# Optimization experiments

Hardware: AMD Instinct MI355X
Metric: run time of the kernel (lower is better)

Reference implementation:

```python
import jax, jax.numpy as jnp
import numpy as np

NUM_BLOCKS = 32
B, S = 8, 2048


def setup_inputs() -> dict:
    key = jax.random.key(0)
    k1, k2, k3 = jax.random.split(key, 3)
    h = jax.random.uniform(k1, (B, S, NUM_BLOCKS, 4), dtype=jnp.float32)
    W = jax.random.uniform(k2, (B, S, NUM_BLOCKS, NUM_BLOCKS), dtype=jnp.float32)
    stim = jax.random.uniform(k3, (B, S, NUM_BLOCKS), dtype=jnp.float32)
    return {"h": h, "W": W, "stim": stim}


def _step(h, W, stim):
    nb = h.shape[-2]
    eye = jnp.eye(nb, dtype=W.dtype)
    W_no_self = W * (1.0 - eye)                      # zero self-connections
    # neighbor inflow: [b,s,i,j] @ [b,s,j,c] -> [b,s,i,c]
    inflow = jnp.einsum('bsij,bsjc->bsic', W_no_self, h)
    total_w = W_no_self.sum(axis=-1, keepdims=True) + 1e-8
    neigh = inflow / total_w                          # weighted neighbor mean

    E, P, G, L = h[..., 0], h[..., 1], h[..., 2], h[..., 3]
    En, Pn, Gn, Ln = neigh[..., 0], neigh[..., 1], neigh[..., 2], neigh[..., 3]

    clamp01 = lambda x: jnp.clip(x, 0.0, 1.0)
    E_new = clamp01(E + 0.3 * stim - 0.4 * P - 0.2 * G)
    P_new = clamp01(P + 0.5 * stim + 0.3 * (Pn - P) - 0.2 * E)
    G_new = clamp01(G + 0.4 * E * (1.0 - P) + 0.2 * (Gn - G) - 0.3 * P)
    good_neighbor = 0.5 * En + 0.5 * Gn
    L_new = clamp01(L + 0.4 * good_neighbor + 0.3 * (Ln - L) - 0.3 * P)

    h_new = jnp.stack([E_new, P_new, G_new, L_new], axis=-1)  # [b,s,nb,4]

    # pairwise euclidean distance over the 4 EPGL channels (torch.cdist p=2)
    diff = h_new[..., :, None, :] - h_new[..., None, :, :]    # [b,s,nb,nb,4]
    sq = jnp.sum(diff * diff, axis=-1)
    # safe sqrt: zero distance -> 0 (matches cdist; avoids nan grads)
    h_diff = jnp.where(sq > 0, jnp.sqrt(jnp.where(sq > 0, sq, 1.0)), 0.0)

    mutual_L = 0.5 * (L_new[..., :, None] + L_new[..., None, :])
    alpha, beta = 0.1 * mutual_L, 0.05
    W_new = W + alpha * h_diff - beta * W
    W_new = jnp.clip(W_new, 0.0, 1.0) * (1.0 - eye)
    return h_new, W_new


def reference(h, W, stim):
    return _step(h, W, stim)
```

## Files before the change

kernel.cpp:

```cpp
#include <hip/hip_runtime.h>

#define NB 32
#define WAVES_PER_BLOCK 4

__device__ __forceinline__ float clamp01(float x) {
    return fminf(fmaxf(x, 0.0f), 1.0f);
}

__global__ __launch_bounds__(256, 8) void biotoken_step(
    const float* __restrict__ h,
    const float* __restrict__ W,
    const float* __restrict__ stim,
    float* __restrict__ out_h,
    float* __restrict__ out_W)
{
    const int lw    = threadIdx.x & 63;
    const int wave  = threadIdx.x >> 6;
    const int token = blockIdx.x * WAVES_PER_BLOCK + wave;
    const int i     = lw & 31;
    const int half  = lw >> 5;
    const int c0    = half * 16;

    __shared__ float s_hin [WAVES_PER_BLOCK][NB * 4];
    __shared__ float s_hnew[WAVES_PER_BLOCK][NB * 4];

    const float*  Wt  = W + (size_t)token * (NB * NB);
    const float4* wrp = (const float4*)(Wt + i * NB + c0);
    float4 wrow[4];
    wrow[0] = wrp[0];
    wrow[1] = wrp[1];
    wrow[2] = wrp[2];
    wrow[3] = wrp[3];

    if (lw < NB) {
        ((float4*)s_hin[wave])[lw] =
            ((const float4*)(h + (size_t)token * (NB * 4)))[lw];
    }
    const float sti = stim[(size_t)token * NB + i];
    __builtin_amdgcn_wave_barrier();

    const float* shin = s_hin[wave];
    const float* wf   = (const float*)wrow;

    float accE = 0.f, accP = 0.f, accG = 0.f, accL = 0.f, tot = 0.f;
    #pragma unroll
    for (int t = 0; t < 16; ++t) {
        const int j = c0 + t;
        float w = wf[t];
        w = (j == i) ? 0.0f : w;
        const float4 hj = *(const float4*)&shin[j * 4];
        accE = fmaf(w, hj.x, accE);
        accP = fmaf(w, hj.y, accP);
        accG = fmaf(w, hj.z, accG);
        accL = fmaf(w, hj.w, accL);
        tot += w;
    }
    accE += __shfl_xor(accE, 32);
    accP += __shfl_xor(accP, 32);
    accG += __shfl_xor(accG, 32);
    accL += __shfl_xor(accL, 32);
    tot  += __shfl_xor(tot,  32);

    const float inv = 1.0f / (tot + 1e-8f);
    const float En = accE * inv, Pn = accP * inv, Gn = accG * inv, Ln = accL * inv;

    const float4 hi = *(const float4*)&shin[i * 4];
    const float E = hi.x, P = hi.y, G = hi.z, L = hi.w;

    const float E_new = clamp01(E + 0.3f * sti - 0.4f * P - 0.2f * G);
    const float P_new = clamp01(P + 0.5f * sti + 0.3f * (Pn - P) - 0.2f * E);
    const float G_new = clamp01(G + 0.4f * E * (1.0f - P) + 0.2f * (Gn - G) - 0.3f * P);
    const float good  = 0.5f * En + 0.5f * Gn;
    const float L_new = clamp01(L + 0.4f * good + 0.3f * (Ln - L) - 0.3f * P);

    const float4 hr = make_float4(E_new, P_new, G_new, L_new);
    if (half == 0) {
        ((float4*)s_hnew[wave])[i] = hr;
        ((float4*)(out_h + (size_t)token * (NB * 4)))[i] = hr;
    }
    __builtin_amdgcn_wave_barrier();

    const float* shn = s_hnew[wave];
    const float  Lr  = hr.w;
    float4* outWr = (float4*)(out_W + (size_t)token * (NB * NB) + i * NB + c0);

    #pragma unroll
    for (int e = 0; e < 4; ++e) {
        float4 res;
        float* resp = &res.x;
        #pragma unroll
        for (int q = 0; q < 4; ++q) {
            const int t = 4 * e + q;
            const int j = c0 + t;
            const float4 hj = *(const float4*)&shn[j * 4];
            const float dx = hr.x - hj.x;
            const float dy = hr.y - hj.y;
            const float dz = hr.z - hj.z;
            const float dw = hr.w - hj.w;
            const float sq = dx * dx + dy * dy + dz * dz + dw * dw;
            const float dist = sqrtf(sq);
            const float mutual = 0.5f * (Lr + hj.w);
            float wn = 0.95f * wf[t] + 0.1f * mutual * dist;
            wn = clamp01(wn);
            resp[q] = (j == i) ? 0.0f : wn;
        }
        outWr[e] = res;
    }
}

extern "C" void kernel_launch(void* const* d_in, const int* in_sizes, int n_in,
                              void* d_out, int out_size, void* d_ws, size_t ws_size,
                              hipStream_t stream) {
    const float* h    = (const float*)d_in[0];
    const float* W    = (const float*)d_in[1];
    const float* stim = (const float*)d_in[2];

    const int tokens = in_sizes[2] / NB;
    float* out_h = (float*)d_out;
    float* out_W = (float*)d_out + (size_t)tokens * NB * 4;

    const int blocks = tokens / WAVES_PER_BLOCK;
    biotoken_step<<<blocks, 256, 0, stream>>>(h, W, stim, out_h, out_W);
}
```

Baseline: 142.9 us.

## Split step into h-update and W-update kernels with coalesced W access

```diff
diff --git a/kernel.cpp b/kernel.cpp
--- a/kernel.cpp
+++ b/kernel.cpp
@@ -1,36 +1,31 @@
 #include <hip/hip_runtime.h>
 
 #define NB 32
-#define WAVES_PER_BLOCK 4
+#define WPB 4
 
 __device__ __forceinline__ float clamp01(float x) {
     return fminf(fmaxf(x, 0.0f), 1.0f);
 }
 
-__global__ __launch_bounds__(256, 8) void biotoken_step(
+__global__ __launch_bounds__(256, 8) void biotoken_hnew(
     const float* __restrict__ h,
     const float* __restrict__ W,
     const float* __restrict__ stim,
-    float* __restrict__ out_h,
-    float* __restrict__ out_W)
+    float* __restrict__ out_h)
 {
     const int lw    = threadIdx.x & 63;
     const int wave  = threadIdx.x >> 6;
-    const int token = blockIdx.x * WAVES_PER_BLOCK + wave;
+    const int token = blockIdx.x * WPB + wave;
     const int i     = lw & 31;
     const int half  = lw >> 5;
     const int c0    = half * 16;
 
-    __shared__ float s_hin [WAVES_PER_BLOCK][NB * 4];
-    __shared__ float s_hnew[WAVES_PER_BLOCK][NB * 4];
+    __shared__ float s_hin[WPB][NB * 4];
 
     const float*  Wt  = W + (size_t)token * (NB * NB);
     const float4* wrp = (const float4*)(Wt + i * NB + c0);
     float4 wrow[4];
-    wrow[0] = wrp[0];
-    wrow[1] = wrp[1];
-    wrow[2] = wrp[2];
-    wrow[3] = wrp[3];
+    wrow[0] = wrp[0]; wrow[1] = wrp[1]; wrow[2] = wrp[2]; wrow[3] = wrp[3];
 
     if (lw < NB) {
         ((float4*)s_hin[wave])[lw] =
@@ -73,26 +68,58 @@
     const float good  = 0.5f * En + 0.5f * Gn;
     const float L_new = clamp01(L + 0.4f * good + 0.3f * (Ln - L) - 0.3f * P);
 
-    const float4 hr = make_float4(E_new, P_new, G_new, L_new);
     if (half == 0) {
-        ((float4*)s_hnew[wave])[i] = hr;
-        ((float4*)(out_h + (size_t)token * (NB * 4)))[i] = hr;
+        ((float4*)(out_h + (size_t)token * (NB * 4)))[i] =
+            make_float4(E_new, P_new, G_new, L_new);
+    }
+}
+
+__global__ __launch_bounds__(256, 6) void biotoken_wnew(
+    const float* __restrict__ W,
+    const float* __restrict__ hn,
+    float* __restrict__ out_W)
+{
+    const int lw    = threadIdx.x & 63;
+    const int wave  = threadIdx.x >> 6;
+    const int token = blockIdx.x * WPB + wave;
+
+    __shared__ float s_hn[WPB][NB * 4];
+
+    const float4* Wt = (const float4*)(W + (size_t)token * (NB * NB));
+    float4 wrs[4];
+    wrs[0] = Wt[0 * 64 + lw];
+    wrs[1] = Wt[1 * 64 + lw];
+    wrs[2] = Wt[2 * 64 + lw];
+    wrs[3] = Wt[3 * 64 + lw];
+
+    if (lw < NB) {
+        ((float4*)s_hn[wave])[lw] =
+            ((const float4*)(hn + (size_t)token * (NB * 4)))[lw];
     }
     __builtin_amdgcn_wave_barrier();
 
-    const float* shn = s_hnew[wave];
-    const float  Lr  = hr.w;
-    float4* outWr = (float4*)(out_W + (size_t)token * (NB * NB) + i * NB + c0);
-
+    const float* shn = s_hn[wave];
+    const int jb0 = (lw & 7) * 4;
+    float4 hjv[4];
     #pragma unroll
     for (int e = 0; e < 4; ++e) {
+        hjv[e] = *(const float4*)&shn[(jb0 + e) * 4];
+    }
+
+    float4* outWt = (float4*)(out_W + (size_t)token * (NB * NB));
+    #pragma unroll
+    for (int k = 0; k < 4; ++k) {
+        const int m = k * 64 + lw;
+        const int r = m >> 3;
+        const float4 hr = *(const float4*)&shn[r * 4];
+        const float  Lr = hr.w;
+        const float* wp = (const float*)&wrs[k];
         float4 res;
         float* resp = &res.x;
         #pragma unroll
-        for (int q = 0; q < 4; ++q) {
-            const int t = 4 * e + q;
-            const int j = c0 + t;
-            const float4 hj = *(const float4*)&shn[j * 4];
+        for (int e = 0; e < 4; ++e) {
+            const int j = jb0 + e;
+            const float4 hj = hjv[e];
             const float dx = hr.x - hj.x;
             const float dy = hr.y - hj.y;
             const float dz = hr.z - hj.z;
@@ -100,11 +127,11 @@
             const float sq = dx * dx + dy * dy + dz * dz + dw * dw;
             const float dist = sqrtf(sq);
             const float mutual = 0.5f * (Lr + hj.w);
-            float wn = 0.95f * wf[t] + 0.1f * mutual * dist;
+            float wn = 0.95f * wp[e] + 0.1f * mutual * dist;
             wn = clamp01(wn);
-            resp[q] = (j == i) ? 0.0f : wn;
+            resp[e] = (j == r) ? 0.0f : wn;
         }
-        outWr[e] = res;
+        outWt[m] = res;
     }
 }
 
@@ -119,6 +146,7 @@
     float* out_h = (float*)d_out;
     float* out_W = (float*)d_out + (size_t)tokens * NB * 4;
 
-    const int blocks = tokens / WAVES_PER_BLOCK;
-    biotoken_step<<<blocks, 256, 0, stream>>>(h, W, stim, out_h, out_W);
+    const int blocks = tokens / WPB;
+    biotoken_hnew<<<blocks, 256, 0, stream>>>(h, W, stim, out_h);
+    biotoken_wnew<<<blocks, 256, 0, stream>>>(W, out_h, out_W);
 }
```

Result: slower. 145.8 us (+2.0%).
